# Kernel tuning notes

Hardware: AMD Instinct MI355X
Metric: run time of the kernel (lower is better)

The kernel has to match this reference:

```python
import jax, jax.numpy as jnp
import numpy as np

N = 50000      # nodes
E = 400000     # edges (before self-loops)
IN = 128
HID = 64
HEADS = 8
OUT = 3
NEG_SLOPE = 0.2
EPS = 1e-6


def setup_inputs() -> dict:
    key = jax.random.key(0)
    ks = jax.random.split(key, 32)
    def nrm(k, shape, s=0.05):
        return jax.random.normal(k, shape, dtype=jnp.float32) * s
    inp = {}
    inp['x'] = nrm(ks[0], (N, IN), 1.0)
    inp['edge_index'] = jax.random.randint(ks[1], (2, E), 0, N)
    inp['res_W'] = nrm(ks[2], (OUT, IN))
    inp['res_b'] = jnp.zeros((OUT,), jnp.float32)
    # (in, out, heads, concat) per GAT layer
    dims = [(IN, HID, HEADS, True), (HID * HEADS, HID, HEADS, True),
            (HID * HEADS, HID, HEADS, True), (HID * HEADS, OUT, 1, False)]
    j = 3
    for i, (ci, co, h, cc) in enumerate(dims):
        inp['ln_g%d' % i] = jnp.ones((ci,), jnp.float32)
        inp['ln_b%d' % i] = jnp.zeros((ci,), jnp.float32)
        inp['W%d' % i] = nrm(ks[j], (h * co, ci)); j += 1
        inp['asr%d' % i] = nrm(ks[j], (h, co)); j += 1
        inp['adt%d' % i] = nrm(ks[j], (h, co)); j += 1
        inp['b%d' % i] = jnp.zeros((h * co if cc else co,), jnp.float32)
    return inp


def layer_norm(x, g, b):
    mu = x.mean(-1, keepdims=True)
    var = ((x - mu) ** 2).mean(-1, keepdims=True)
    return (x - mu) / jnp.sqrt(var + EPS) * g + b


def gat_conv(x, src, dst, W, a_src, a_dst, bias, heads, co, concat):
    n = x.shape[0]
    h = (x @ W.T).reshape(n, heads, co)                    # [N,H,C]
    al_src = jnp.sum(h * a_src, axis=-1)                   # [N,H]
    al_dst = jnp.sum(h * a_dst, axis=-1)                   # [N,H]
    e = jax.nn.leaky_relu(al_src[src] + al_dst[dst], NEG_SLOPE)  # [E',H]
    # segment softmax over incoming edges of each destination node
    m = jax.ops.segment_max(e, dst, num_segments=n)
    e = jnp.exp(e - m[dst])
    s = jax.ops.segment_sum(e, dst, num_segments=n)
    alpha = e / s[dst]                                     # [E',H]
    msg = h[src] * alpha[..., None]                        # [E',H,C]
    out = jax.ops.segment_sum(msg, dst, num_segments=n)    # [N,H,C]
    out = out.reshape(n, heads * co) if concat else out.mean(axis=1)
    return out + bias


def reference(x, edge_index, res_W, res_b,
              ln_g0, ln_b0, W0, asr0, adt0, b0,
              ln_g1, ln_b1, W1, asr1, adt1, b1,
              ln_g2, ln_b2, W2, asr2, adt2, b2,
              ln_g3, ln_b3, W3, asr3, adt3, b3):
    n = x.shape[0]
    loops = jnp.arange(n)
    src = jnp.concatenate([edge_index[0], loops])          # add self-loops (PyG default)
    dst = jnp.concatenate([edge_index[1], loops])
    residual = x @ res_W.T + res_b
    layers = [(ln_g0, ln_b0, W0, asr0, adt0, b0, HEADS, HID, True),
              (ln_g1, ln_b1, W1, asr1, adt1, b1, HEADS, HID, True),
              (ln_g2, ln_b2, W2, asr2, adt2, b2, HEADS, HID, True),
              (ln_g3, ln_b3, W3, asr3, adt3, b3, 1, OUT, False)]
    h = x
    num_layers = len(layers)
    for i, (g, bb, W, a_s, a_d, bi, hd, co, cc) in enumerate(layers):
        x_res = h
        h = layer_norm(h, g, bb)
        h = gat_conv(h, src, dst, W, a_s, a_d, bi, hd, co, cc)
        if i < num_layers - 1:
            h = jax.nn.gelu(h, approximate=False)
            if h.shape == x_res.shape:
                h = h + x_res
    return h + residual
```

## Files before the change

### kernel.cpp

```cpp
#include <hip/hip_runtime.h>
#include <math.h>

#define NN 50000
#define MPAD 50048
#define EE 400000
#define NE 450000
#define IN_F 128
#define NEG_SLOPE 0.2f
#define EPSV 1e-6f

typedef unsigned short bf16u;
typedef short bf8_t __attribute__((ext_vector_type(8)));
typedef float f32x4 __attribute__((ext_vector_type(4)));

__device__ __forceinline__ float bf2f(unsigned int u) {
    return __uint_as_float(u << 16);
}
__device__ __forceinline__ float bf2f_hi(unsigned int u) {
    return __uint_as_float(u & 0xFFFF0000u);
}
__device__ __forceinline__ bf16u f2bf(float f) {
    unsigned int u = __float_as_uint(f);
    unsigned int r = (u + 0x7FFFu + ((u >> 16) & 1u)) >> 16;
    return (bf16u)r;
}
__device__ __forceinline__ float gelu_f(float v) {
    return 0.5f * v * (1.0f + erff(v * 0.70710678118654752f));
}
__device__ __forceinline__ float lrelu(float v) {
    return fmaxf(v, NEG_SLOPE * v);
}

__device__ __forceinline__ void gload_lds16(const void* g, void* l) {
    __builtin_amdgcn_global_load_lds(
        (__attribute__((address_space(1))) void*)(g),
        (__attribute__((address_space(3))) void*)(l), 16, 0, 0);
}

__global__ void k_zero_i32(int* p, int n) {
    int i = blockIdx.x * 256 + threadIdx.x;
    if (i < n) p[i] = 0;
}

__global__ void k_deg(const int* __restrict__ ei, int* __restrict__ deg) {
    int i = blockIdx.x * 256 + threadIdx.x;
    if (i >= NE) return;
    int d = (i < EE) ? ei[EE + i] : (i - EE);
    atomicAdd(&deg[d], 1);
}

__global__ __launch_bounds__(256) void k_scan1(const int* __restrict__ deg,
                                               int* __restrict__ incl,
                                               int* __restrict__ bsums, int n) {
    __shared__ int sm[1024];
    int base = blockIdx.x * 1024;
    for (int i = threadIdx.x; i < 1024; i += 256)
        sm[i] = (base + i < n) ? deg[base + i] : 0;
    __syncthreads();
    for (int off = 1; off < 1024; off <<= 1) {
        int v[4];
#pragma unroll
        for (int j = 0; j < 4; j++) {
            int i = threadIdx.x + 256 * j;
            v[j] = (i >= off) ? sm[i - off] : 0;
        }
        __syncthreads();
#pragma unroll
        for (int j = 0; j < 4; j++) {
            int i = threadIdx.x + 256 * j;
            sm[i] += v[j];
        }
        __syncthreads();
    }
    for (int i = threadIdx.x; i < 1024; i += 256)
        if (base + i < n) incl[base + i] = sm[i];
    if (threadIdx.x == 0) bsums[blockIdx.x] = sm[1023];
}

__global__ void k_scan2(int* bsums, int nb) {
    if (threadIdx.x == 0 && blockIdx.x == 0) {
        int run = 0;
        for (int i = 0; i < nb; i++) { int v = bsums[i]; bsums[i] = run; run += v; }
    }
}

__global__ void k_scan3(const int* __restrict__ deg, int* __restrict__ rowptr,
                        int* __restrict__ cursor, const int* __restrict__ bsums,
                        int n, int ne) {
    int i = blockIdx.x * 256 + threadIdx.x;
    if (i < n) {
        int excl = rowptr[i] + bsums[i >> 10] - deg[i];
        rowptr[i] = excl;
        cursor[i] = excl;
    }
    if (i == n) rowptr[n] = ne;
}

__global__ void k_scatter(const int* __restrict__ ei, int* __restrict__ cursor,
                          int* __restrict__ col) {
    int i = blockIdx.x * 256 + threadIdx.x;
    if (i >= NE) return;
    int s, d;
    if (i < EE) { s = ei[i]; d = ei[EE + i]; }
    else        { s = i - EE; d = i - EE; }
    int p = atomicAdd(&cursor[d], 1);
    col[p] = s;
}

__global__ void k_cast3(const float* __restrict__ w0, bf16u* __restrict__ o0,
                        const float* __restrict__ w1, bf16u* __restrict__ o1,
                        const float* __restrict__ w2, bf16u* __restrict__ o2) {
    int i = blockIdx.x * 256 + threadIdx.x;
    if (i < 65536) { o0[i] = f2bf(w0[i]); return; }
    i -= 65536;
    if (i < 262144) { o1[i] = f2bf(w1[i]); return; }
    i -= 262144;
    if (i < 262144) o2[i] = f2bf(w2[i]);
}

__global__ __launch_bounds__(256) void k_castres2(const float* __restrict__ x,
                                                  const float* __restrict__ rw,
                                                  const float* __restrict__ rb,
                                                  const float* __restrict__ g0,
                                                  const float* __restrict__ b0,
                                                  bf16u* __restrict__ abuf,
                                                  float* __restrict__ res, int n) {
    int row = (blockIdx.x * 256 + threadIdx.x) >> 6;
    int lane = threadIdx.x & 63;
    if (row >= n) return;
    float2 v = *(const float2*)(x + (size_t)row * 128 + lane * 2);
    float2 w0 = *(const float2*)(rw + 0 * 128 + lane * 2);
    float2 w1 = *(const float2*)(rw + 1 * 128 + lane * 2);
    float2 w2 = *(const float2*)(rw + 2 * 128 + lane * 2);
    float s = v.x + v.y, s2 = v.x * v.x + v.y * v.y;
    float a0 = v.x * w0.x + v.y * w0.y;
    float a1 = v.x * w1.x + v.y * w1.y;
    float a2 = v.x * w2.x + v.y * w2.y;
#pragma unroll
    for (int off = 32; off; off >>= 1) {
        s  += __shfl_xor(s, off);
        s2 += __shfl_xor(s2, off);
        a0 += __shfl_xor(a0, off);
        a1 += __shfl_xor(a1, off);
        a2 += __shfl_xor(a2, off);
    }
    float mu = s * (1.0f / 128.0f);
    float var = s2 * (1.0f / 128.0f) - mu * mu;
    float rs = rsqrtf(var + EPSV);
    float2 gg = *(const float2*)(g0 + lane * 2);
    float2 bb = *(const float2*)(b0 + lane * 2);
    float l0 = fmaf((v.x - mu) * rs, gg.x, bb.x);
    float l1 = fmaf((v.y - mu) * rs, gg.y, bb.y);
    *(unsigned int*)(abuf + (size_t)row * 128 + lane * 2) =
        (unsigned int)f2bf(l0) | ((unsigned int)f2bf(l1) << 16);
    if (lane == 0) {
        res[row * 3 + 0] = a0 + rb[0];
        res[row * 3 + 1] = a1 + rb[1];
        res[row * 3 + 2] = a2 + rb[2];
    }
}

#define BM 128
#define BN 128
#define BK2 64
__global__ __launch_bounds__(256) void k_gemm_db(const bf16u* __restrict__ A,
                                                 const bf16u* __restrict__ Wb,
                                                 bf16u* __restrict__ C,
                                                 const float* __restrict__ asr,
                                                 const float* __restrict__ adt,
                                                 float* __restrict__ alsrc,
                                                 float* __restrict__ aldst,
                                                 int Mreal, int ci, int K) {
    __shared__ __align__(16) bf16u As[2][BM * BK2];
    __shared__ __align__(16) bf16u Bs[2][BN * BK2];
    const int tid = threadIdx.x;
    const int w = tid >> 6, lane = tid & 63;
    const int row0 = blockIdx.y * BM, col0 = blockIdx.x * BN;
    const int wr = (w >> 1) * 64, wc = (w & 1) * 64;

    const int lrow = lane >> 3;
    const int scolx = ((lane & 7) * 8) ^ (lrow << 3);
    const bf16u* gA = A + (size_t)(row0 + w * 32 + lrow) * ci + scolx;
    const bf16u* gB = Wb + (size_t)(col0 + w * 32 + lrow) * ci + scolx;

    const int nk = ci / BK2;

#pragma unroll
    for (int j = 0; j < 4; j++) {
        gload_lds16(gA + (size_t)(j * 8) * ci, &As[0][(w * 32 + j * 8) * BK2]);
        gload_lds16(gB + (size_t)(j * 8) * ci, &Bs[0][(w * 32 + j * 8) * BK2]);
    }
    __syncthreads();

    f32x4 acc[4][4] = {};
    const int fr = lane & 15;
    const int fk = (lane >> 4) * 8;
    const int fxor = (fr & 7) << 3;

    for (int t = 0; t < nk; t++) {
        const int cur = t & 1;
        if (t + 1 < nk) {
            const int k0 = (t + 1) * BK2;
#pragma unroll
            for (int j = 0; j < 4; j++) {
                gload_lds16(gA + (size_t)(j * 8) * ci + k0, &As[cur ^ 1][(w * 32 + j * 8) * BK2]);
                gload_lds16(gB + (size_t)(j * 8) * ci + k0, &Bs[cur ^ 1][(w * 32 + j * 8) * BK2]);
            }
        }
#pragma unroll
        for (int ks = 0; ks < 2; ks++) {
            bf8_t af[4], bfv[4];
#pragma unroll
            for (int m = 0; m < 4; m++)
                af[m] = *(const bf8_t*)&As[cur][(wr + m * 16 + fr) * BK2 + ((ks * 32 + fk) ^ fxor)];
#pragma unroll
            for (int n = 0; n < 4; n++)
                bfv[n] = *(const bf8_t*)&Bs[cur][(wc + n * 16 + fr) * BK2 + ((ks * 32 + fk) ^ fxor)];
#pragma unroll
            for (int m = 0; m < 4; m++)
#pragma unroll
                for (int n = 0; n < 4; n++)
                    acc[m][n] = __builtin_amdgcn_mfma_f32_16x16x32_bf16(af[m], bfv[n], acc[m][n], 0, 0, 0);
        }
        if (t + 1 < nk) __syncthreads();
    }

    const int fc = lane & 15;
    const int fq = (lane >> 4) * 4;

#pragma unroll
    for (int m = 0; m < 4; m++) {
#pragma unroll
        for (int r = 0; r < 4; r++) {
            int row = row0 + wr + m * 16 + fq + r;
            if (row >= Mreal) continue;
#pragma unroll
            for (int n = 0; n < 4; n++) {
                int col = col0 + wc + n * 16 + fc;
                C[(size_t)row * K + col] = f2bf(acc[m][n][r]);
            }
        }
    }

    const int head = blockIdx.x * 2 + (wc >> 6);
    float av[4], dv[4];
#pragma unroll
    for (int n = 0; n < 4; n++) {
        av[n] = asr[head * 64 + n * 16 + fc];
        dv[n] = adt[head * 64 + n * 16 + fc];
    }
#pragma unroll
    for (int m = 0; m < 4; m++) {
#pragma unroll
        for (int r = 0; r < 4; r++) {
            float s1 = acc[m][0][r] * av[0] + acc[m][1][r] * av[1]
                     + acc[m][2][r] * av[2] + acc[m][3][r] * av[3];
            float s2 = acc[m][0][r] * dv[0] + acc[m][1][r] * dv[1]
                     + acc[m][2][r] * dv[2] + acc[m][3][r] * dv[3];
#pragma unroll
            for (int o = 1; o < 16; o <<= 1) {
                s1 += __shfl_xor(s1, o);
                s2 += __shfl_xor(s2, o);
            }
            int row = row0 + wr + m * 16 + fq + r;
            if (fc == 0 && row < Mreal) {
                alsrc[row * 8 + head] = s1;
                aldst[row * 8 + head] = s2;
            }
        }
    }
}

__global__ __launch_bounds__(256) void k_lin3b(const bf16u* __restrict__ an,
                                               const float* __restrict__ W,
                                               const float* __restrict__ a_s,
                                               const float* __restrict__ a_d,
                                               bf16u* __restrict__ hlin3,
                                               float* __restrict__ alsrc,
                                               float* __restrict__ aldst, int n) {
    int row = (blockIdx.x * 256 + threadIdx.x) >> 6;
    int lane = threadIdx.x & 63;
    if (row >= n) return;
    uint4 r = *(const uint4*)(an + (size_t)row * 512 + lane * 8);
    unsigned int u[4] = {r.x, r.y, r.z, r.w};
    float ln[8];
#pragma unroll
    for (int j = 0; j < 4; j++) {
        ln[2 * j]     = bf2f(u[j] & 0xFFFFu);
        ln[2 * j + 1] = bf2f_hi(u[j]);
    }
    float a0 = 0.f, a1 = 0.f, a2 = 0.f;
#pragma unroll
    for (int j = 0; j < 8; j++) {
        int k = lane * 8 + j;
        a0 += ln[j] * W[k];
        a1 += ln[j] * W[512 + k];
        a2 += ln[j] * W[1024 + k];
    }
#pragma unroll
    for (int off = 32; off; off >>= 1) {
        a0 += __shfl_down(a0, off);
        a1 += __shfl_down(a1, off);
        a2 += __shfl_down(a2, off);
    }
    if (lane == 0) {
        *(unsigned int*)(hlin3 + (size_t)row * 4) =
            (unsigned int)f2bf(a0) | ((unsigned int)f2bf(a1) << 16);
        *(unsigned int*)(hlin3 + (size_t)row * 4 + 2) = (unsigned int)f2bf(a2);
        alsrc[row] = a0 * a_s[0] + a1 * a_s[1] + a2 * a_s[2];
        aldst[row] = a0 * a_d[0] + a1 * a_d[1] + a2 * a_d[2];
    }
}

__global__ __launch_bounds__(256) void k_aggN2(const bf16u* __restrict__ hlin,
                                               const float* __restrict__ alsrc,
                                               const float* __restrict__ aldst,
                                               const int* __restrict__ rowptr,
                                               const int* __restrict__ col,
                                               const float* __restrict__ bias,
                                               bf16u* __restrict__ hio,
                                               const float* __restrict__ gn,
                                               const float* __restrict__ bn,
                                               bf16u* __restrict__ abuf,
                                               int n, int dores) {
    __shared__ uint2 aldsU[4][8][66];
    int wv = threadIdx.x >> 6;
    int node = (blockIdx.x * 256 + threadIdx.x) >> 6;
    int lane = threadIdx.x & 63;
    if (node >= n) return;
    int beg = rowptr[node], end = rowptr[node + 1];
    int deg = end - beg;

    const float4* dvv = (const float4*)(aldst + node * 8);
    float4 da = dvv[0], db = dvv[1];
    float ad[8] = {da.x, da.y, da.z, da.w, db.x, db.y, db.z, db.w};

    float s = 0.f, s2 = 0.f;
    float fin[8];

    if (deg <= 64) {
        unsigned int offb = 0;
        float ex[8];
        if (lane < deg) {
            int srcreg = col[beg + lane];
            offb = (unsigned int)srcreg << 10;
            const float4* sv = (const float4*)(alsrc + srcreg * 8);
            float4 sa = sv[0], sb = sv[1];
            float sl[8] = {sa.x, sa.y, sa.z, sa.w, sb.x, sb.y, sb.z, sb.w};
#pragma unroll
            for (int h = 0; h < 8; h++) ex[h] = __expf(lrelu(sl[h] + ad[h]));
        } else {
#pragma unroll
            for (int h = 0; h < 8; h++) ex[h] = 0.f;
        }
#pragma unroll
        for (int h = 0; h < 8; h++) {
            uint2 t;
            t.x = __float_as_uint(ex[h]);
            t.y = offb;
            aldsU[wv][h][lane] = t;
        }
        asm volatile("s_waitcnt lgkmcnt(0)" ::: "memory");

        int hl = lane >> 3, s8 = lane & 7;
        const uint2* hrow = &aldsU[wv][hl][0];
        float ps = 0.f;
#pragma unroll
        for (int k2 = 0; k2 < 4; k2++) {
            uint4 q = *(const uint4*)(hrow + s8 * 8 + k2 * 2);
            ps += __uint_as_float(q.x) + __uint_as_float(q.z);
        }
#pragma unroll
        for (int o = 1; o < 8; o <<= 1) ps += __shfl_xor(ps, o);
        float invs = 1.0f / ps;

        const uint2* myal = hrow;
        const char* base2 = (const char*)hlin + (lane << 4);
        float acc[8] = {};
        int e = 0;
        for (; e + 2 <= deg; e += 2) {
            uint2 t0 = myal[e];
            uint2 t1 = myal[e + 1];
            uint4 u0 = *(const uint4*)(base2 + t0.y);
            uint4 u1 = *(const uint4*)(base2 + t1.y);
            float a0 = __uint_as_float(t0.x) * invs;
            float a1 = __uint_as_float(t1.x) * invs;
            acc[0] = fmaf(a0, bf2f(u0.x & 0xFFFFu), acc[0]);
            acc[1] = fmaf(a0, bf2f_hi(u0.x),        acc[1]);
            acc[2] = fmaf(a0, bf2f(u0.y & 0xFFFFu), acc[2]);
            acc[3] = fmaf(a0, bf2f_hi(u0.y),        acc[3]);
            acc[4] = fmaf(a0, bf2f(u0.z & 0xFFFFu), acc[4]);
            acc[5] = fmaf(a0, bf2f_hi(u0.z),        acc[5]);
            acc[6] = fmaf(a0, bf2f(u0.w & 0xFFFFu), acc[6]);
            acc[7] = fmaf(a0, bf2f_hi(u0.w),        acc[7]);
            acc[0] = fmaf(a1, bf2f(u1.x & 0xFFFFu), acc[0]);
            acc[1] = fmaf(a1, bf2f_hi(u1.x),        acc[1]);
            acc[2] = fmaf(a1, bf2f(u1.y & 0xFFFFu), acc[2]);
            acc[3] = fmaf(a1, bf2f_hi(u1.y),        acc[3]);
            acc[4] = fmaf(a1, bf2f(u1.z & 0xFFFFu), acc[4]);
            acc[5] = fmaf(a1, bf2f_hi(u1.z),        acc[5]);
            acc[6] = fmaf(a1, bf2f(u1.w & 0xFFFFu), acc[6]);
            acc[7] = fmaf(a1, bf2f_hi(u1.w),        acc[7]);
        }
        if (e < deg) {
            uint2 t0 = myal[e];
            uint4 u0 = *(const uint4*)(base2 + t0.y);
            float a0 = __uint_as_float(t0.x) * invs;
            acc[0] = fmaf(a0, bf2f(u0.x & 0xFFFFu), acc[0]);
            acc[1] = fmaf(a0, bf2f_hi(u0.x),        acc[1]);
            acc[2] = fmaf(a0, bf2f(u0.y & 0xFFFFu), acc[2]);
            acc[3] = fmaf(a0, bf2f_hi(u0.y),        acc[3]);
            acc[4] = fmaf(a0, bf2f(u0.z & 0xFFFFu), acc[4]);
            acc[5] = fmaf(a0, bf2f_hi(u0.z),        acc[5]);
            acc[6] = fmaf(a0, bf2f(u0.w & 0xFFFFu), acc[6]);
            acc[7] = fmaf(a0, bf2f_hi(u0.w),        acc[7]);
        }

        size_t idx = (size_t)node * 512 + lane * 8;
        float4 b0 = *(const float4*)(bias + lane * 8);
        float4 b1 = *(const float4*)(bias + lane * 8 + 4);
        float bb[8] = {b0.x, b0.y, b0.z, b0.w, b1.x, b1.y, b1.z, b1.w};
#pragma unroll
        for (int j = 0; j < 8; j++) fin[j] = gelu_f(acc[j] + bb[j]);
        if (dores) {
            uint4 up = *(const uint4*)(hio + idx);
            fin[0] += bf2f(up.x & 0xFFFFu); fin[1] += bf2f_hi(up.x);
            fin[2] += bf2f(up.y & 0xFFFFu); fin[3] += bf2f_hi(up.y);
            fin[4] += bf2f(up.z & 0xFFFFu); fin[5] += bf2f_hi(up.z);
            fin[6] += bf2f(up.w & 0xFFFFu); fin[7] += bf2f_hi(up.w);
        }
        uint4 pk;
        pk.x = (unsigned int)f2bf(fin[0]) | ((unsigned int)f2bf(fin[1]) << 16);
        pk.y = (unsigned int)f2bf(fin[2]) | ((unsigned int)f2bf(fin[3]) << 16);
        pk.z = (unsigned int)f2bf(fin[4]) | ((unsigned int)f2bf(fin[5]) << 16);
        pk.w = (unsigned int)f2bf(fin[6]) | ((unsigned int)f2bf(fin[7]) << 16);
        *(uint4*)(hio + idx) = pk;
#pragma unroll
        for (int j = 0; j < 8; j++) { s += fin[j]; s2 += fin[j] * fin[j]; }

#pragma unroll
        for (int off = 32; off; off >>= 1) {
            s  += __shfl_xor(s, off);
            s2 += __shfl_xor(s2, off);
        }
        float mu = s * (1.0f / 512.0f);
        float rs = rsqrtf(s2 * (1.0f / 512.0f) - mu * mu + EPSV);
        float4 g0 = *(const float4*)(gn + lane * 8);
        float4 g1 = *(const float4*)(gn + lane * 8 + 4);
        float4 n0 = *(const float4*)(bn + lane * 8);
        float4 n1 = *(const float4*)(bn + lane * 8 + 4);
        float gg[8] = {g0.x, g0.y, g0.z, g0.w, g1.x, g1.y, g1.z, g1.w};
        float nb[8] = {n0.x, n0.y, n0.z, n0.w, n1.x, n1.y, n1.z, n1.w};
        float lnv[8];
#pragma unroll
        for (int j = 0; j < 8; j++) lnv[j] = fmaf((fin[j] - mu) * rs, gg[j], nb[j]);
        uint4 pl;
        pl.x = (unsigned int)f2bf(lnv[0]) | ((unsigned int)f2bf(lnv[1]) << 16);
        pl.y = (unsigned int)f2bf(lnv[2]) | ((unsigned int)f2bf(lnv[3]) << 16);
        pl.z = (unsigned int)f2bf(lnv[4]) | ((unsigned int)f2bf(lnv[5]) << 16);
        pl.w = (unsigned int)f2bf(lnv[6]) | ((unsigned int)f2bf(lnv[7]) << 16);
        *(uint4*)(abuf + idx) = pl;
    } else {
        float fins[8];
        for (int h = 0; h < 8; h++) {
            float adh = ad[h];
            float m = -INFINITY;
            for (int e = beg + lane; e < end; e += 64)
                m = fmaxf(m, lrelu(alsrc[col[e] * 8 + h] + adh));
#pragma unroll
            for (int off = 32; off; off >>= 1) m = fmaxf(m, __shfl_xor(m, off));
            float sum = 0.f;
            for (int e = beg + lane; e < end; e += 64)
                sum += __expf(lrelu(alsrc[col[e] * 8 + h] + adh) - m);
#pragma unroll
            for (int off = 32; off; off >>= 1) sum += __shfl_xor(sum, off);
            float inv = 1.0f / sum;
            float acc = 0.f;
            for (int e = beg; e < end; e++) {
                int src = col[e];
                float alpha = __expf(lrelu(alsrc[src * 8 + h] + adh) - m) * inv;
                acc = fmaf(alpha, bf2f(hlin[((size_t)src << 9) + h * 64 + lane]), acc);
            }
            float fv = gelu_f(acc + bias[h * 64 + lane]);
            size_t idx = (size_t)node * 512 + h * 64 + lane;
            if (dores) fv += bf2f(hio[idx]);
            hio[idx] = f2bf(fv);
            fins[h] = fv;
            s += fv; s2 += fv * fv;
        }
#pragma unroll
        for (int off = 32; off; off >>= 1) {
            s  += __shfl_xor(s, off);
            s2 += __shfl_xor(s2, off);
        }
        float mu = s * (1.0f / 512.0f);
        float rs = rsqrtf(s2 * (1.0f / 512.0f) - mu * mu + EPSV);
        for (int h = 0; h < 8; h++) {
            int c = h * 64 + lane;
            abuf[(size_t)node * 512 + c] = f2bf(fmaf((fins[h] - mu) * rs, gn[c], bn[c]));
        }
    }
}

__global__ __launch_bounds__(256) void k_aggF(const bf16u* __restrict__ hlin3,
                                              const float* __restrict__ alsrc,
                                              const float* __restrict__ aldst,
                                              const int* __restrict__ rowptr,
                                              const int* __restrict__ col,
                                              const float* __restrict__ bias,
                                              float* __restrict__ outf,
                                              const float* __restrict__ resid, int n) {
    int node = (blockIdx.x * 256 + threadIdx.x) >> 6;
    int lane = threadIdx.x & 63;
    if (node >= n) return;
    int beg = rowptr[node], end = rowptr[node + 1];
    int deg = end - beg;
    float adh = aldst[node];

    if (deg <= 64) {
        int src = 0;
        float raw = -INFINITY;
        if (lane < deg) {
            src = col[beg + lane];
            raw = lrelu(alsrc[src] + adh);
        }
        float m = raw;
#pragma unroll
        for (int off = 32; off; off >>= 1) m = fmaxf(m, __shfl_xor(m, off));
        float ex = (lane < deg) ? __expf(raw - m) : 0.f;
        float sum = ex;
#pragma unroll
        for (int off = 32; off; off >>= 1) sum += __shfl_xor(sum, off);
        float alpha = ex / sum;

        float c0 = 0.f, c1 = 0.f, c2 = 0.f;
        if (lane < deg) {
            uint2 u = *(const uint2*)(hlin3 + (size_t)src * 4);
            c0 = alpha * bf2f(u.x & 0xFFFFu);
            c1 = alpha * bf2f_hi(u.x);
            c2 = alpha * bf2f(u.y & 0xFFFFu);
        }
#pragma unroll
        for (int off = 32; off; off >>= 1) {
            c0 += __shfl_xor(c0, off);
            c1 += __shfl_xor(c1, off);
            c2 += __shfl_xor(c2, off);
        }
        if (lane == 0) {
            outf[node * 3 + 0] = c0 + bias[0] + resid[node * 3 + 0];
            outf[node * 3 + 1] = c1 + bias[1] + resid[node * 3 + 1];
            outf[node * 3 + 2] = c2 + bias[2] + resid[node * 3 + 2];
        }
    } else {
        float m = -INFINITY;
        for (int e = beg + lane; e < end; e += 64)
            m = fmaxf(m, lrelu(alsrc[col[e]] + adh));
#pragma unroll
        for (int off = 32; off; off >>= 1) m = fmaxf(m, __shfl_xor(m, off));
        float sum = 0.f;
        for (int e = beg + lane; e < end; e += 64)
            sum += __expf(lrelu(alsrc[col[e]] + adh) - m);
#pragma unroll
        for (int off = 32; off; off >>= 1) sum += __shfl_xor(sum, off);
        float inv = 1.0f / sum;
        float acc = 0.f;
        for (int e = beg; e < end; e++) {
            int src = col[e];
            float alpha = __expf(lrelu(alsrc[src] + adh) - m) * inv;
            if (lane < 3) acc += alpha * bf2f(hlin3[(size_t)src * 4 + lane]);
        }
        if (lane < 3)
            outf[node * 3 + lane] = acc + bias[lane] + resid[node * 3 + lane];
    }
}

extern "C" void kernel_launch(void* const* d_in, const int* in_sizes, int n_in,
                              void* d_out, int out_size, void* d_ws, size_t ws_size,
                              hipStream_t stream) {
    const float* x    = (const float*)d_in[0];
    const int*   ei   = (const int*)d_in[1];
    const float* resW = (const float*)d_in[2];
    const float* resb = (const float*)d_in[3];
    const float *lng[4], *lnb[4], *Wm[4], *asr[4], *adt[4], *bias[4];
    int idx = 4;
    for (int i = 0; i < 4; i++) {
        lng[i]  = (const float*)d_in[idx++];
        lnb[i]  = (const float*)d_in[idx++];
        Wm[i]   = (const float*)d_in[idx++];
        asr[i]  = (const float*)d_in[idx++];
        adt[i]  = (const float*)d_in[idx++];
        bias[i] = (const float*)d_in[idx++];
    }

    char* base = (char*)d_ws;
    size_t off = 0;
    auto alloc = [&](size_t bytes) {
        void* p = base + off;
        off += (bytes + 255) & ~(size_t)255;
        return p;
    };
    float* alsrc = (float*)alloc((size_t)NN * 8 * 4);
    float* aldst = (float*)alloc((size_t)NN * 8 * 4);
    float* resid = (float*)alloc((size_t)NN * 3 * 4);
    int* rowptr  = (int*)alloc((size_t)(NN + 1) * 4);
    int* cursor  = (int*)alloc((size_t)NN * 4);
    int* deg     = (int*)alloc((size_t)NN * 4);
    int* colidx  = (int*)alloc((size_t)NE * 4);
    int* bsums   = (int*)alloc(256 * 4);
    bf16u* wb0   = (bf16u*)alloc((size_t)512 * 128 * 2);
    bf16u* wb1   = (bf16u*)alloc((size_t)512 * 512 * 2);
    bf16u* wb2   = (bf16u*)alloc((size_t)512 * 512 * 2);
    bf16u* hbuf  = (bf16u*)alloc((size_t)MPAD * 512 * 2);
    bf16u* lbuf  = (bf16u*)alloc((size_t)MPAD * 512 * 2);
    bf16u* abuf  = (bf16u*)alloc((size_t)MPAD * 512 * 2);
    if (off > ws_size) return;

    float* out = (float*)d_out;

    k_zero_i32<<<(NN + 255) / 256, 256, 0, stream>>>(deg, NN);
    k_deg<<<(NE + 255) / 256, 256, 0, stream>>>(ei, deg);
    int nb = (NN + 1023) / 1024;
    k_scan1<<<nb, 256, 0, stream>>>(deg, rowptr, bsums, NN);
    k_scan2<<<1, 64, 0, stream>>>(bsums, nb);
    k_scan3<<<(NN + 1 + 255) / 256, 256, 0, stream>>>(deg, rowptr, cursor, bsums, NN, NE);
    k_scatter<<<(NE + 255) / 256, 256, 0, stream>>>(ei, cursor, colidx);

    int rowBlocks = (NN * 64 + 255) / 256;
    k_cast3<<<(589824 + 255) / 256, 256, 0, stream>>>(Wm[0], wb0, Wm[1], wb1, Wm[2], wb2);

    const bf16u* wb[3] = {wb0, wb1, wb2};
    const int ci_a[3] = {128, 512, 512};
    dim3 ggrid(512 / BN, MPAD / BM);

    k_castres2<<<rowBlocks, 256, 0, stream>>>(x, resW, resb, lng[0], lnb[0],
                                              abuf, resid, NN);
    for (int i = 0; i < 3; i++) {
        int dores = (i >= 1) ? 1 : 0;
        k_gemm_db<<<ggrid, 256, 0, stream>>>(abuf, wb[i], lbuf,
                                             asr[i], adt[i], alsrc, aldst,
                                             NN, ci_a[i], 512);
        k_aggN2<<<rowBlocks, 256, 0, stream>>>(lbuf, alsrc, aldst, rowptr, colidx,
                                               bias[i], hbuf, lng[i + 1], lnb[i + 1],
                                               abuf, NN, dores);
    }
    k_lin3b<<<rowBlocks, 256, 0, stream>>>(abuf, Wm[3], asr[3], adt[3],
                                           lbuf, alsrc, aldst, NN);
    k_aggF<<<rowBlocks, 256, 0, stream>>>(lbuf, alsrc, aldst, rowptr, colidx,
                                          bias[3], out, resid, NN);
}
```

Baseline: 647.4 us.

## Single-buffer GEMM, unroll aggregation by four, skip dead writes and softmax max

The GEMM goes from double-buffered LDS to single-buffered loads with a sync before and after each K tile, which halves LDS use and may raise occupancy but gives up load/compute overlap. The neighbour aggregation loop is unrolled to four edges with two accumulator sets, to get more gathers in flight. The last hidden layer no longer writes its residual output, since nothing reads it. The final-layer softmax drops the max subtraction, which saves a wave reduction but risks overflow for large logits.

```diff
diff --git a/kernel.cpp b/kernel.cpp
--- a/kernel.cpp
+++ b/kernel.cpp
@@ -29,6 +29,16 @@
 }
 __device__ __forceinline__ float lrelu(float v) {
     return fmaxf(v, NEG_SLOPE * v);
+}
+__device__ __forceinline__ void fma8(float* acc, float a, uint4 u) {
+    acc[0] = fmaf(a, bf2f(u.x & 0xFFFFu), acc[0]);
+    acc[1] = fmaf(a, bf2f_hi(u.x),        acc[1]);
+    acc[2] = fmaf(a, bf2f(u.y & 0xFFFFu), acc[2]);
+    acc[3] = fmaf(a, bf2f_hi(u.y),        acc[3]);
+    acc[4] = fmaf(a, bf2f(u.z & 0xFFFFu), acc[4]);
+    acc[5] = fmaf(a, bf2f_hi(u.z),        acc[5]);
+    acc[6] = fmaf(a, bf2f(u.w & 0xFFFFu), acc[6]);
+    acc[7] = fmaf(a, bf2f_hi(u.w),        acc[7]);
 }
 
 __device__ __forceinline__ void gload_lds16(const void* g, void* l) {
@@ -163,7 +173,7 @@
 #define BM 128
 #define BN 128
 #define BK2 64
-__global__ __launch_bounds__(256) void k_gemm_db(const bf16u* __restrict__ A,
+__global__ __launch_bounds__(256) void k_gemm_sb(const bf16u* __restrict__ A,
                                                  const bf16u* __restrict__ Wb,
                                                  bf16u* __restrict__ C,
                                                  const float* __restrict__ asr,
@@ -171,8 +181,8 @@
                                                  float* __restrict__ alsrc,
                                                  float* __restrict__ aldst,
                                                  int Mreal, int ci, int K) {
-    __shared__ __align__(16) bf16u As[2][BM * BK2];
-    __shared__ __align__(16) bf16u Bs[2][BN * BK2];
+    __shared__ __align__(16) bf16u As[BM * BK2];
+    __shared__ __align__(16) bf16u Bs[BN * BK2];
     const int tid = threadIdx.x;
     const int w = tid >> 6, lane = tid & 63;
     const int row0 = blockIdx.y * BM, col0 = blockIdx.x * BN;
@@ -185,44 +195,35 @@
 
     const int nk = ci / BK2;
 
-#pragma unroll
-    for (int j = 0; j < 4; j++) {
-        gload_lds16(gA + (size_t)(j * 8) * ci, &As[0][(w * 32 + j * 8) * BK2]);
-        gload_lds16(gB + (size_t)(j * 8) * ci, &Bs[0][(w * 32 + j * 8) * BK2]);
-    }
-    __syncthreads();
-
     f32x4 acc[4][4] = {};
     const int fr = lane & 15;
     const int fk = (lane >> 4) * 8;
     const int fxor = (fr & 7) << 3;
 
     for (int t = 0; t < nk; t++) {
-        const int cur = t & 1;
-        if (t + 1 < nk) {
-            const int k0 = (t + 1) * BK2;
-#pragma unroll
-            for (int j = 0; j < 4; j++) {
-                gload_lds16(gA + (size_t)(j * 8) * ci + k0, &As[cur ^ 1][(w * 32 + j * 8) * BK2]);
-                gload_lds16(gB + (size_t)(j * 8) * ci + k0, &Bs[cur ^ 1][(w * 32 + j * 8) * BK2]);
-            }
-        }
+        if (t) __syncthreads();
+        const int k0 = t * BK2;
+#pragma unroll
+        for (int j = 0; j < 4; j++) {
+            gload_lds16(gA + (size_t)(j * 8) * ci + k0, &As[(w * 32 + j * 8) * BK2]);
+            gload_lds16(gB + (size_t)(j * 8) * ci + k0, &Bs[(w * 32 + j * 8) * BK2]);
+        }
+        __syncthreads();
 #pragma unroll
         for (int ks = 0; ks < 2; ks++) {
             bf8_t af[4], bfv[4];
 #pragma unroll
             for (int m = 0; m < 4; m++)
-                af[m] = *(const bf8_t*)&As[cur][(wr + m * 16 + fr) * BK2 + ((ks * 32 + fk) ^ fxor)];
+                af[m] = *(const bf8_t*)&As[(wr + m * 16 + fr) * BK2 + ((ks * 32 + fk) ^ fxor)];
 #pragma unroll
             for (int n = 0; n < 4; n++)
-                bfv[n] = *(const bf8_t*)&Bs[cur][(wc + n * 16 + fr) * BK2 + ((ks * 32 + fk) ^ fxor)];
+                bfv[n] = *(const bf8_t*)&Bs[(wc + n * 16 + fr) * BK2 + ((ks * 32 + fk) ^ fxor)];
 #pragma unroll
             for (int m = 0; m < 4; m++)
 #pragma unroll
                 for (int n = 0; n < 4; n++)
                     acc[m][n] = __builtin_amdgcn_mfma_f32_16x16x32_bf16(af[m], bfv[n], acc[m][n], 0, 0, 0);
         }
-        if (t + 1 < nk) __syncthreads();
     }
 
     const int fc = lane & 15;
@@ -322,7 +323,7 @@
                                                const float* __restrict__ gn,
                                                const float* __restrict__ bn,
                                                bf16u* __restrict__ abuf,
-                                               int n, int dores) {
+                                               int n, int dores, int wrh) {
     __shared__ uint2 aldsU[4][8][66];
     int wv = threadIdx.x >> 6;
     int node = (blockIdx.x * 256 + threadIdx.x) >> 6;
@@ -376,44 +377,35 @@
 
         const uint2* myal = hrow;
         const char* base2 = (const char*)hlin + (lane << 4);
-        float acc[8] = {};
+        float acc0[8] = {}, acc1[8] = {};
         int e = 0;
-        for (; e + 2 <= deg; e += 2) {
+        for (; e + 4 <= deg; e += 4) {
+            uint2 t0 = myal[e];
+            uint2 t1 = myal[e + 1];
+            uint2 t2 = myal[e + 2];
+            uint2 t3 = myal[e + 3];
+            uint4 u0 = *(const uint4*)(base2 + t0.y);
+            uint4 u1 = *(const uint4*)(base2 + t1.y);
+            uint4 u2 = *(const uint4*)(base2 + t2.y);
+            uint4 u3 = *(const uint4*)(base2 + t3.y);
+            fma8(acc0, __uint_as_float(t0.x) * invs, u0);
+            fma8(acc1, __uint_as_float(t1.x) * invs, u1);
+            fma8(acc0, __uint_as_float(t2.x) * invs, u2);
+            fma8(acc1, __uint_as_float(t3.x) * invs, u3);
+        }
+        if (e + 2 <= deg) {
             uint2 t0 = myal[e];
             uint2 t1 = myal[e + 1];
             uint4 u0 = *(const uint4*)(base2 + t0.y);
             uint4 u1 = *(const uint4*)(base2 + t1.y);
-            float a0 = __uint_as_float(t0.x) * invs;
-            float a1 = __uint_as_float(t1.x) * invs;
-            acc[0] = fmaf(a0, bf2f(u0.x & 0xFFFFu), acc[0]);
-            acc[1] = fmaf(a0, bf2f_hi(u0.x),        acc[1]);
-            acc[2] = fmaf(a0, bf2f(u0.y & 0xFFFFu), acc[2]);
-            acc[3] = fmaf(a0, bf2f_hi(u0.y),        acc[3]);
-            acc[4] = fmaf(a0, bf2f(u0.z & 0xFFFFu), acc[4]);
-            acc[5] = fmaf(a0, bf2f_hi(u0.z),        acc[5]);
-            acc[6] = fmaf(a0, bf2f(u0.w & 0xFFFFu), acc[6]);
-            acc[7] = fmaf(a0, bf2f_hi(u0.w),        acc[7]);
-            acc[0] = fmaf(a1, bf2f(u1.x & 0xFFFFu), acc[0]);
-            acc[1] = fmaf(a1, bf2f_hi(u1.x),        acc[1]);
-            acc[2] = fmaf(a1, bf2f(u1.y & 0xFFFFu), acc[2]);
-            acc[3] = fmaf(a1, bf2f_hi(u1.y),        acc[3]);
-            acc[4] = fmaf(a1, bf2f(u1.z & 0xFFFFu), acc[4]);
-            acc[5] = fmaf(a1, bf2f_hi(u1.z),        acc[5]);
-            acc[6] = fmaf(a1, bf2f(u1.w & 0xFFFFu), acc[6]);
-            acc[7] = fmaf(a1, bf2f_hi(u1.w),        acc[7]);
+            fma8(acc0, __uint_as_float(t0.x) * invs, u0);
+            fma8(acc1, __uint_as_float(t1.x) * invs, u1);
+            e += 2;
         }
         if (e < deg) {
             uint2 t0 = myal[e];
             uint4 u0 = *(const uint4*)(base2 + t0.y);
-            float a0 = __uint_as_float(t0.x) * invs;
-            acc[0] = fmaf(a0, bf2f(u0.x & 0xFFFFu), acc[0]);
-            acc[1] = fmaf(a0, bf2f_hi(u0.x),        acc[1]);
-            acc[2] = fmaf(a0, bf2f(u0.y & 0xFFFFu), acc[2]);
-            acc[3] = fmaf(a0, bf2f_hi(u0.y),        acc[3]);
-            acc[4] = fmaf(a0, bf2f(u0.z & 0xFFFFu), acc[4]);
-            acc[5] = fmaf(a0, bf2f_hi(u0.z),        acc[5]);
-            acc[6] = fmaf(a0, bf2f(u0.w & 0xFFFFu), acc[6]);
-            acc[7] = fmaf(a0, bf2f_hi(u0.w),        acc[7]);
+            fma8(acc0, __uint_as_float(t0.x) * invs, u0);
         }
 
         size_t idx = (size_t)node * 512 + lane * 8;
@@ -421,7 +413,7 @@
         float4 b1 = *(const float4*)(bias + lane * 8 + 4);
         float bb[8] = {b0.x, b0.y, b0.z, b0.w, b1.x, b1.y, b1.z, b1.w};
 #pragma unroll
-        for (int j = 0; j < 8; j++) fin[j] = gelu_f(acc[j] + bb[j]);
+        for (int j = 0; j < 8; j++) fin[j] = gelu_f(acc0[j] + acc1[j] + bb[j]);
         if (dores) {
             uint4 up = *(const uint4*)(hio + idx);
             fin[0] += bf2f(up.x & 0xFFFFu); fin[1] += bf2f_hi(up.x);
@@ -429,12 +421,14 @@
             fin[4] += bf2f(up.z & 0xFFFFu); fin[5] += bf2f_hi(up.z);
             fin[6] += bf2f(up.w & 0xFFFFu); fin[7] += bf2f_hi(up.w);
         }
-        uint4 pk;
-        pk.x = (unsigned int)f2bf(fin[0]) | ((unsigned int)f2bf(fin[1]) << 16);
-        pk.y = (unsigned int)f2bf(fin[2]) | ((unsigned int)f2bf(fin[3]) << 16);
-        pk.z = (unsigned int)f2bf(fin[4]) | ((unsigned int)f2bf(fin[5]) << 16);
-        pk.w = (unsigned int)f2bf(fin[6]) | ((unsigned int)f2bf(fin[7]) << 16);
-        *(uint4*)(hio + idx) = pk;
+        if (wrh) {
+            uint4 pk;
+            pk.x = (unsigned int)f2bf(fin[0]) | ((unsigned int)f2bf(fin[1]) << 16);
+            pk.y = (unsigned int)f2bf(fin[2]) | ((unsigned int)f2bf(fin[3]) << 16);
+            pk.z = (unsigned int)f2bf(fin[4]) | ((unsigned int)f2bf(fin[5]) << 16);
+            pk.w = (unsigned int)f2bf(fin[6]) | ((unsigned int)f2bf(fin[7]) << 16);
+            *(uint4*)(hio + idx) = pk;
+        }
 #pragma unroll
         for (int j = 0; j < 8; j++) { s += fin[j]; s2 += fin[j] * fin[j]; }
 
@@ -484,7 +478,7 @@
             float fv = gelu_f(acc + bias[h * 64 + lane]);
             size_t idx = (size_t)node * 512 + h * 64 + lane;
             if (dores) fv += bf2f(hio[idx]);
-            hio[idx] = f2bf(fv);
+            if (wrh) hio[idx] = f2bf(fv);
             fins[h] = fv;
             s += fv; s2 += fv * fv;
         }
@@ -519,15 +513,11 @@
 
     if (deg <= 64) {
         int src = 0;
-        float raw = -INFINITY;
+        float ex = 0.f;
         if (lane < deg) {
             src = col[beg + lane];
-            raw = lrelu(alsrc[src] + adh);
-        }
-        float m = raw;
-#pragma unroll
-        for (int off = 32; off; off >>= 1) m = fmaxf(m, __shfl_xor(m, off));
-        float ex = (lane < deg) ? __expf(raw - m) : 0.f;
+            ex = __expf(lrelu(alsrc[src] + adh));
+        }
         float sum = ex;
 #pragma unroll
         for (int off = 32; off; off >>= 1) sum += __shfl_xor(sum, off);
@@ -636,12 +626,13 @@
                                               abuf, resid, NN);
     for (int i = 0; i < 3; i++) {
         int dores = (i >= 1) ? 1 : 0;
-        k_gemm_db<<<ggrid, 256, 0, stream>>>(abuf, wb[i], lbuf,
+        int wrh = (i < 2) ? 1 : 0;
+        k_gemm_sb<<<ggrid, 256, 0, stream>>>(abuf, wb[i], lbuf,
                                              asr[i], adt[i], alsrc, aldst,
                                              NN, ci_a[i], 512);
         k_aggN2<<<rowBlocks, 256, 0, stream>>>(lbuf, alsrc, aldst, rowptr, colidx,
                                                bias[i], hbuf, lng[i + 1], lnb[i + 1],
-                                               abuf, NN, dores);
+                                               abuf, NN, dores, wrh);
     }
     k_lin3b<<<rowBlocks, 256, 0, stream>>>(abuf, Wm[3], asr[3], adt[3],
                                            lbuf, alsrc, aldst, NN);
```

Result: no change. 640.2 us (-1.1%).
